# Kernel tuning notes

Hardware: AMD Instinct MI355X
Metric: run time of the kernel (lower is better)

## Reference

```python
import jax, jax.numpy as jnp
import numpy as np

SIGMA = 1.0  # init kwarg sigma

def _rbf_kernel(A):
    # K[i,j] = exp(-0.5 * ||a_i - a_j||^2 / sigma^2)
    sq = jnp.sum(A * A, axis=1)                      # [n]
    d2 = sq[:, None] + sq[None, :] - 2.0 * (A @ A.T)  # [n, n]
    return jnp.exp(-0.5 * d2 / (SIGMA ** 2))

def _double_center(K):
    # C K C with C = I - 11^T/n, done in O(n^2) via mean subtraction
    row = K.mean(axis=1, keepdims=True)
    col = K.mean(axis=0, keepdims=True)
    tot = K.mean()
    return K - row - col + tot

def setup_inputs() -> dict:
    key = jax.random.key(0)
    kx, ky = jax.random.split(key)
    X = jax.random.normal(kx, (4096, 512), dtype=jnp.float32)
    Y = jax.random.normal(ky, (4096, 512), dtype=jnp.float32)
    return {"X": X, "Y": Y}

def reference(X, Y):
    n = X.shape[0]
    KXc = _double_center(_rbf_kernel(X))
    KYc = _double_center(_rbf_kernel(Y))
    # trace(KX C KY C) = sum(center(KX) * center(KY)) since K symmetric, C idempotent
    hsic = jnp.sum(KXc * KYc) / ((n - 1) ** 2)
    return hsic
```

## Files before the change

### kernel.cpp

```cpp
#include <hip/hip_runtime.h>
#include <hip/hip_bf16.h>

namespace {

constexpr int N = 4096;
constexpr int D = 512;
constexpr int BM = 128;
constexpr int BK = 64;
constexpr int KITERS = D / BK;
constexpr int NB = N / BM;
constexpr int NBLK = NB * (NB + 1) / 2;
constexpr int TILEB = BM * BK;
constexpr int PANELB = BM * D;

constexpr size_t OFF_XB  = 0;
constexpr size_t OFF_YB  = (size_t)N * D;
constexpr size_t OFF_SQX = OFF_YB + (size_t)N * D;
constexpr size_t OFF_SQY = OFF_SQX + (size_t)N * 4;
constexpr size_t OFF_SX  = OFF_SQY + (size_t)N * 4;
constexpr size_t OFF_SY  = OFF_SX + (size_t)N * 4;
constexpr size_t OFF_T1  = OFF_SY + (size_t)N * 4;
constexpr size_t WS_NEED = OFF_T1 + 4;


constexpr float D2_SKIP = 240.f;

typedef __attribute__((ext_vector_type(4))) float floatx4;
typedef __attribute__((ext_vector_type(2))) long longx2;

__device__ inline void stage16(const void* g, void* l) {
  __builtin_amdgcn_global_load_lds(
      (const __attribute__((address_space(1))) unsigned int*)g,
      (__attribute__((address_space(3))) unsigned int*)l, 16, 0, 0);
}

__device__ inline unsigned short bf16bits(float f) {
  return __builtin_bit_cast(unsigned short, __float2bfloat16(f));
}

__global__ void prep_kernel(const float* __restrict__ X, const float* __restrict__ Y,
                            unsigned char* __restrict__ Xf8, unsigned char* __restrict__ Yf8,
                            float* __restrict__ sqX, float* __restrict__ sqY,
                            float* __restrict__ sX, float* __restrict__ sY,
                            float* __restrict__ T1) {
  const int wave = threadIdx.x >> 6, lane = threadIdx.x & 63;
  const int row = blockIdx.x * 4 + wave;
  const int m = blockIdx.y;
  const float* __restrict__ src = m ? Y : X;
  unsigned char* __restrict__ dst = m ? Yf8 : Xf8;
  float* __restrict__ dsq = m ? sqY : sqX;

  if (threadIdx.x < 4) {
    float* z = m ? sY : sX;
    z[blockIdx.x * 4 + threadIdx.x] = 0.f;
  }
  if (blockIdx.x == 0 && m == 0 && threadIdx.x == 0) *T1 = 0.f;

  const float4* s4 = (const float4*)(src + (size_t)row * D);
  float4 v0 = s4[lane * 2];
  float4 v1 = s4[lane * 2 + 1];
  float acc = v0.x * v0.x + v0.y * v0.y + v0.z * v0.z + v0.w * v0.w
            + v1.x * v1.x + v1.y * v1.y + v1.z * v1.z + v1.w * v1.w;

  unsigned int w0 = 0, w1 = 0;
  w0 = __builtin_amdgcn_cvt_pk_fp8_f32(v0.x, v0.y, w0, false);
  w0 = __builtin_amdgcn_cvt_pk_fp8_f32(v0.z, v0.w, w0, true);
  w1 = __builtin_amdgcn_cvt_pk_fp8_f32(v1.x, v1.y, w1, false);
  w1 = __builtin_amdgcn_cvt_pk_fp8_f32(v1.z, v1.w, w1, true);
  const unsigned long long pk =
      (unsigned long long)w0 | ((unsigned long long)w1 << 32);

  const int p    = row >> 7;
  const int half = (row >> 6) & 1;
  const int nib  = (row >> 4) & 3;
  const int cl   = row & 15;
  const int ks   = lane >> 3;
  const int pass = (lane >> 2) & 1;
  const int quad = lane & 3;
  const size_t off = (size_t)p * PANELB + (size_t)ks * TILEB +
                     half * 4096 + nib * 1024 + quad * 256 + cl * 16 + pass * 8;
  *(unsigned long long*)(dst + off) = pk;

#pragma unroll
  for (int mm = 32; mm >= 1; mm >>= 1) acc += __shfl_xor(acc, mm, 64);
  if (lane == 0) dsq[row] = acc;
}

__launch_bounds__(256, 3)
__global__ void hsic_main(const unsigned char* __restrict__ Xf8,
                          const unsigned char* __restrict__ Yf8,
                          const float* __restrict__ sqX, const float* __restrict__ sqY,
                          float* __restrict__ sX, float* __restrict__ sY,
                          float* __restrict__ T1) {
  __shared__ __align__(16) unsigned char smem[2][2 * TILEB];

  const int b = blockIdx.x;
  int idx = (b & 7) * (NBLK / 8) + (b >> 3);

  const float nf = (float)NB + 0.5f;
  int bI = (int)(nf - sqrtf(nf * nf - 2.0f * (float)idx));
  if (bI < 0) bI = 0;
  if (bI >= NB) bI = NB - 1;
  while (bI * NB - bI * (bI - 1) / 2 > idx) --bI;
  while ((bI + 1) * NB - (bI + 1) * bI / 2 <= idx) ++bI;
  const int bJ = bI + (idx - (bI * NB - bI * (bI - 1) / 2));
  const bool offdiag = (bI != bJ);

  const int tid = threadIdx.x;
  const int lane = tid & 63, wave = tid >> 6;
  const int wm = wave >> 1, wn = wave & 1;
  const int quad = lane >> 4, cl = lane & 15;

  const unsigned char* gAx = Xf8 + (size_t)bI * PANELB;
  const unsigned char* gBx = Xf8 + (size_t)bJ * PANELB;
  const unsigned char* gAy = Yf8 + (size_t)bI * PANELB;
  const unsigned char* gBy = Yf8 + (size_t)bJ * PANELB;

  floatx4 acc[4][4];
#pragma unroll
  for (int i = 0; i < 4; ++i)
#pragma unroll
    for (int j = 0; j < 4; ++j) acc[i][j] = (floatx4){0.f, 0.f, 0.f, 0.f};

  auto stage_all = [&](int iter, int buf) {
    const unsigned char* gA = (iter < KITERS) ? gAx : gAy;
    const unsigned char* gB = (iter < KITERS) ? gBx : gBy;
    const size_t ks0 = (size_t)(iter & (KITERS - 1)) * TILEB;
#pragma unroll
    for (int h = 0; h < 2; ++h) {
      const int c = tid + h * 256;
      const size_t goff = ks0 + (size_t)c * 16;
      stage16(gA + goff, &smem[buf][0 * TILEB + c * 16]);
      if (offdiag) stage16(gB + goff, &smem[buf][1 * TILEB + c * 16]);
    }
  };

  const int Ib = bI * BM + wm * 64;
  const int Jb = bJ * BM + wn * 64;

  unsigned int kxp[4][4][2];
  unsigned int fmask = 0;
  float t1l = 0.f;

  stage_all(0, 0);

  for (int iter = 0; iter < 2 * KITERS; ++iter) {
    const int buf = iter & 1;
    __syncthreads();
    if (iter + 1 < 2 * KITERS) stage_all(iter + 1, buf ^ 1);

    const unsigned char* A = &smem[buf][0];
    const unsigned char* B = offdiag ? &smem[buf][TILEB] : &smem[buf][0];

    longx2 bf[4];
#pragma unroll
    for (int ni = 0; ni < 4; ++ni)
      bf[ni] = *(const longx2*)&B[wn * 4096 + ni * 1024 + (lane << 4)];
#pragma unroll
    for (int mi = 0; mi < 4; ++mi) {
      const longx2 af = *(const longx2*)&A[wm * 4096 + mi * 1024 + (lane << 4)];
#pragma unroll
      for (int ni = 0; ni < 4; ++ni) {
        acc[mi][ni] = __builtin_amdgcn_mfma_f32_16x16x32_fp8_fp8(af[0], bf[ni][0], acc[mi][ni], 0, 0, 0);
        acc[mi][ni] = __builtin_amdgcn_mfma_f32_16x16x32_fp8_fp8(af[1], bf[ni][1], acc[mi][ni], 0, 0, 0);
      }
    }

    if (iter == KITERS - 1) {
      float rx[4][4];
      float cx[4];
#pragma unroll
      for (int mi = 0; mi < 4; ++mi)
#pragma unroll
        for (int r = 0; r < 4; ++r) rx[mi][r] = 0.f;
#pragma unroll
      for (int ni = 0; ni < 4; ++ni) cx[ni] = 0.f;

#pragma unroll
      for (int mi = 0; mi < 4; ++mi) {
        const int ig0 = Ib + mi * 16 + quad * 4;
        float sxi[4];
#pragma unroll
        for (int r = 0; r < 4; ++r) sxi[r] = sqX[ig0 + r];
#pragma unroll
        for (int ni = 0; ni < 4; ++ni) {
          const int jg = Jb + ni * 16 + cl;
          const float sxj = sqX[jg];
          float d2x[4];
          bool lflag = false;
#pragma unroll
          for (int r = 0; r < 4; ++r) {
            const int ig = ig0 + r;
            d2x[r] = sxi[r] + sxj - 2.f * acc[mi][ni][r];
            lflag |= (d2x[r] < D2_SKIP) | (ig == jg);
          }
          float kxv[4] = {0.f, 0.f, 0.f, 0.f};
          if (__any(lflag)) {
            fmask |= (1u << (mi * 4 + ni));
#pragma unroll
            for (int r = 0; r < 4; ++r) {
              const int ig = ig0 + r;
              kxv[r] = (ig == jg) ? 1.f : __expf(-0.5f * d2x[r]);
              rx[mi][r] += kxv[r];
              cx[ni] += kxv[r];
            }
          }
          kxp[mi][ni][0] = (unsigned)bf16bits(kxv[0]) | ((unsigned)bf16bits(kxv[1]) << 16);
          kxp[mi][ni][1] = (unsigned)bf16bits(kxv[2]) | ((unsigned)bf16bits(kxv[3]) << 16);
          acc[mi][ni] = (floatx4){0.f, 0.f, 0.f, 0.f};
        }
      }

      if (fmask != 0) {
#pragma unroll
        for (int mi = 0; mi < 4; ++mi)
#pragma unroll
          for (int r = 0; r < 4; ++r) {
            float vx = rx[mi][r];
#pragma unroll
            for (int mm = 1; mm < 16; mm <<= 1) vx += __shfl_xor(vx, mm, 16);
            rx[mi][r] = vx;
          }
        if (cl == 0) {
#pragma unroll
          for (int mi = 0; mi < 4; ++mi)
#pragma unroll
            for (int r = 0; r < 4; ++r)
              atomicAdd(&sX[Ib + mi * 16 + quad * 4 + r], rx[mi][r]);
        }
        if (offdiag) {
#pragma unroll
          for (int ni = 0; ni < 4; ++ni) {
            float vx = cx[ni];
            vx += __shfl_xor(vx, 16, 64);
            vx += __shfl_xor(vx, 32, 64);
            if (quad == 0) atomicAdd(&sX[Jb + ni * 16 + cl], vx);
          }
        }
      }
    }
  }

  {
    float ry[4][4];
    float cy[4];
    bool anyy = false;
#pragma unroll
    for (int mi = 0; mi < 4; ++mi)
#pragma unroll
      for (int r = 0; r < 4; ++r) ry[mi][r] = 0.f;
#pragma unroll
    for (int ni = 0; ni < 4; ++ni) cy[ni] = 0.f;

#pragma unroll
    for (int mi = 0; mi < 4; ++mi) {
      const int ig0 = Ib + mi * 16 + quad * 4;
      float syi[4];
#pragma unroll
      for (int r = 0; r < 4; ++r) syi[r] = sqY[ig0 + r];
#pragma unroll
      for (int ni = 0; ni < 4; ++ni) {
        const int jg = Jb + ni * 16 + cl;
        const float syj = sqY[jg];
        float d2y[4];
        bool lflag = false;
#pragma unroll
        for (int r = 0; r < 4; ++r) {
          const int ig = ig0 + r;
          d2y[r] = syi[r] + syj - 2.f * acc[mi][ni][r];
          lflag |= (d2y[r] < D2_SKIP) | (ig == jg);
        }
        const bool xb = (fmask >> (mi * 4 + ni)) & 1u;
        if (__any(lflag) || xb) {
          anyy = true;
          float kyv[4];
#pragma unroll
          for (int r = 0; r < 4; ++r) {
            const int ig = ig0 + r;
            kyv[r] = (ig == jg) ? 1.f : __expf(-0.5f * d2y[r]);
            ry[mi][r] += kyv[r];
            cy[ni] += kyv[r];
          }
          if (xb) {
            const float kx0 = __builtin_bit_cast(float, (kxp[mi][ni][0] & 0xFFFFu) << 16);
            const float kx1 = __builtin_bit_cast(float, kxp[mi][ni][0] & 0xFFFF0000u);
            const float kx2 = __builtin_bit_cast(float, (kxp[mi][ni][1] & 0xFFFFu) << 16);
            const float kx3 = __builtin_bit_cast(float, kxp[mi][ni][1] & 0xFFFF0000u);
            t1l += kx0 * kyv[0] + kx1 * kyv[1] + kx2 * kyv[2] + kx3 * kyv[3];
          }
        }
      }
    }

    if (anyy) {
#pragma unroll
      for (int mi = 0; mi < 4; ++mi)
#pragma unroll
        for (int r = 0; r < 4; ++r) {
          float vy = ry[mi][r];
#pragma unroll
          for (int mm = 1; mm < 16; mm <<= 1) vy += __shfl_xor(vy, mm, 16);
          ry[mi][r] = vy;
        }
      if (cl == 0) {
#pragma unroll
        for (int mi = 0; mi < 4; ++mi)
#pragma unroll
          for (int r = 0; r < 4; ++r)
            atomicAdd(&sY[Ib + mi * 16 + quad * 4 + r], ry[mi][r]);
      }
      if (offdiag) {
#pragma unroll
        for (int ni = 0; ni < 4; ++ni) {
          float vy = cy[ni];
          vy += __shfl_xor(vy, 16, 64);
          vy += __shfl_xor(vy, 32, 64);
          if (quad == 0) atomicAdd(&sY[Jb + ni * 16 + cl], vy);
        }
      }
    }
  }

  if (fmask != 0) {
    t1l *= offdiag ? 2.f : 1.f;
#pragma unroll
    for (int mm = 1; mm < 64; mm <<= 1) t1l += __shfl_xor(t1l, mm, 64);
  }
  __shared__ float tred[4];
  if (lane == 0) tred[wave] = t1l;
  __syncthreads();
  if (tid == 0) {
    const float t = tred[0] + tred[1] + tred[2] + tred[3];
    if (t != 0.f) atomicAdd(T1, t);
  }
}

__global__ void final_kernel(const float* __restrict__ sX, const float* __restrict__ sY,
                             const float* __restrict__ T1, float* __restrict__ out) {
  const int tid = threadIdx.x;
  float dp = 0.f, sa = 0.f, sb = 0.f;
  for (int i = tid; i < N; i += 256) {
    float a = sX[i], b = sY[i];
    dp += a * b; sa += a; sb += b;
  }
#pragma unroll
  for (int mm = 1; mm < 64; mm <<= 1) {
    dp += __shfl_xor(dp, mm, 64);
    sa += __shfl_xor(sa, mm, 64);
    sb += __shfl_xor(sb, mm, 64);
  }
  __shared__ float r0[4], r1[4], r2[4];
  if ((tid & 63) == 0) { int w = tid >> 6; r0[w] = dp; r1[w] = sa; r2[w] = sb; }
  __syncthreads();
  if (tid == 0) {
    dp = r0[0] + r0[1] + r0[2] + r0[3];
    sa = r1[0] + r1[1] + r1[2] + r1[3];
    sb = r2[0] + r2[1] + r2[2] + r2[3];
    const float n = (float)N;
    const float total = T1[0] - (2.f / n) * dp + (sa * sb) / (n * n);
    out[0] = total / ((n - 1.f) * (n - 1.f));
  }
}

}

extern "C" void kernel_launch(void* const* d_in, const int* in_sizes, int n_in,
                              void* d_out, int out_size, void* d_ws, size_t ws_size,
                              hipStream_t stream) {
  const float* X = (const float*)d_in[0];
  const float* Y = (const float*)d_in[1];
  char* ws = (char*)d_ws;
  if (ws_size < WS_NEED) return;

  unsigned char* Xf8 = (unsigned char*)(ws + OFF_XB);
  unsigned char* Yf8 = (unsigned char*)(ws + OFF_YB);
  float* sqX = (float*)(ws + OFF_SQX);
  float* sqY = (float*)(ws + OFF_SQY);
  float* sX  = (float*)(ws + OFF_SX);
  float* sY  = (float*)(ws + OFF_SY);
  float* T1  = (float*)(ws + OFF_T1);
  float* out = (float*)d_out;

  prep_kernel<<<dim3(N / 4, 2), 256, 0, stream>>>(X, Y, Xf8, Yf8, sqX, sqY, sX, sY, T1);
  hsic_main<<<NBLK, 256, 0, stream>>>(Xf8, Yf8, sqX, sqY, sX, sY, T1);
  final_kernel<<<1, 256, 0, stream>>>(sX, sY, T1, out);
}
```

Measured before the change: 96.92 us.

## Stage four K-slices per barrier without double buffering in HSIC main kernel

Replaces the double-buffered 64-wide K pipeline (16 iterations) with 4 iterations that each load 256 bytes of K per row into a single 64KB shared buffer and then compute four slices back to back. This cuts the number of barriers and loop overhead. In exchange, loads no longer overlap with compute, because each iteration waits for its staging to finish. The larger LDS footprint also lowers the launch-bounds occupancy target from 3 to 2 blocks per CU.

```diff
diff --git a/kernel.cpp b/kernel.cpp
--- a/kernel.cpp
+++ b/kernel.cpp
@@ -6,12 +6,12 @@
 constexpr int N = 4096;
 constexpr int D = 512;
 constexpr int BM = 128;
-constexpr int BK = 64;
-constexpr int KITERS = D / BK;
 constexpr int NB = N / BM;
 constexpr int NBLK = NB * (NB + 1) / 2;
-constexpr int TILEB = BM * BK;
+constexpr int TILEB = BM * 64;
 constexpr int PANELB = BM * D;
+constexpr int SLICES = 4;
+constexpr int STAGEB = SLICES * TILEB;
 
 constexpr size_t OFF_XB  = 0;
 constexpr size_t OFF_YB  = (size_t)N * D;
@@ -86,13 +86,14 @@
   if (lane == 0) dsq[row] = acc;
 }
 
-__launch_bounds__(256, 3)
+__launch_bounds__(256, 2)
 __global__ void hsic_main(const unsigned char* __restrict__ Xf8,
                           const unsigned char* __restrict__ Yf8,
                           const float* __restrict__ sqX, const float* __restrict__ sqY,
                           float* __restrict__ sX, float* __restrict__ sY,
                           float* __restrict__ T1) {
-  __shared__ __align__(16) unsigned char smem[2][2 * TILEB];
+  __shared__ __align__(16) unsigned char smem[2 * STAGEB];
+  __shared__ float tred[4];
 
   const int b = blockIdx.x;
   int idx = (b & 7) * (NBLK / 8) + (b >> 3);
@@ -122,16 +123,16 @@
 #pragma unroll
     for (int j = 0; j < 4; ++j) acc[i][j] = (floatx4){0.f, 0.f, 0.f, 0.f};
 
-  auto stage_all = [&](int iter, int buf) {
-    const unsigned char* gA = (iter < KITERS) ? gAx : gAy;
-    const unsigned char* gB = (iter < KITERS) ? gBx : gBy;
-    const size_t ks0 = (size_t)(iter & (KITERS - 1)) * TILEB;
-#pragma unroll
-    for (int h = 0; h < 2; ++h) {
+  auto stage_all = [&](int iter) {
+    const unsigned char* gA = (iter < 2) ? gAx : gAy;
+    const unsigned char* gB = (iter < 2) ? gBx : gBy;
+    const size_t ks0 = (size_t)(iter & 1) * STAGEB;
+#pragma unroll
+    for (int h = 0; h < 8; ++h) {
       const int c = tid + h * 256;
       const size_t goff = ks0 + (size_t)c * 16;
-      stage16(gA + goff, &smem[buf][0 * TILEB + c * 16]);
-      if (offdiag) stage16(gB + goff, &smem[buf][1 * TILEB + c * 16]);
+      stage16(gA + goff, &smem[c * 16]);
+      if (offdiag) stage16(gB + goff, &smem[STAGEB + c * 16]);
     }
   };
 
@@ -142,31 +143,33 @@
   unsigned int fmask = 0;
   float t1l = 0.f;
 
-  stage_all(0, 0);
-
-  for (int iter = 0; iter < 2 * KITERS; ++iter) {
-    const int buf = iter & 1;
+  for (int iter = 0; iter < 4; ++iter) {
+    if (iter > 0) __syncthreads();
+    stage_all(iter);
     __syncthreads();
-    if (iter + 1 < 2 * KITERS) stage_all(iter + 1, buf ^ 1);
-
-    const unsigned char* A = &smem[buf][0];
-    const unsigned char* B = offdiag ? &smem[buf][TILEB] : &smem[buf][0];
-
-    longx2 bf[4];
-#pragma unroll
-    for (int ni = 0; ni < 4; ++ni)
-      bf[ni] = *(const longx2*)&B[wn * 4096 + ni * 1024 + (lane << 4)];
-#pragma unroll
-    for (int mi = 0; mi < 4; ++mi) {
-      const longx2 af = *(const longx2*)&A[wm * 4096 + mi * 1024 + (lane << 4)];
-#pragma unroll
-      for (int ni = 0; ni < 4; ++ni) {
-        acc[mi][ni] = __builtin_amdgcn_mfma_f32_16x16x32_fp8_fp8(af[0], bf[ni][0], acc[mi][ni], 0, 0, 0);
-        acc[mi][ni] = __builtin_amdgcn_mfma_f32_16x16x32_fp8_fp8(af[1], bf[ni][1], acc[mi][ni], 0, 0, 0);
-      }
-    }
-
-    if (iter == KITERS - 1) {
+
+    const unsigned char* A = &smem[0];
+    const unsigned char* B = offdiag ? &smem[STAGEB] : &smem[0];
+
+#pragma unroll
+    for (int s = 0; s < SLICES; ++s) {
+      const int sb = s * TILEB;
+      longx2 bf[4];
+#pragma unroll
+      for (int ni = 0; ni < 4; ++ni)
+        bf[ni] = *(const longx2*)&B[sb + wn * 4096 + ni * 1024 + (lane << 4)];
+#pragma unroll
+      for (int mi = 0; mi < 4; ++mi) {
+        const longx2 af = *(const longx2*)&A[sb + wm * 4096 + mi * 1024 + (lane << 4)];
+#pragma unroll
+        for (int ni = 0; ni < 4; ++ni) {
+          acc[mi][ni] = __builtin_amdgcn_mfma_f32_16x16x32_fp8_fp8(af[0], bf[ni][0], acc[mi][ni], 0, 0, 0);
+          acc[mi][ni] = __builtin_amdgcn_mfma_f32_16x16x32_fp8_fp8(af[1], bf[ni][1], acc[mi][ni], 0, 0, 0);
+        }
+      }
+    }
+
+    if (iter == 1) {
       float rx[4][4];
       float cx[4];
 #pragma unroll
@@ -326,7 +329,6 @@
 #pragma unroll
     for (int mm = 1; mm < 64; mm <<= 1) t1l += __shfl_xor(t1l, mm, 64);
   }
-  __shared__ float tred[4];
   if (lane == 0) tred[wave] = t1l;
   __syncthreads();
   if (tid == 0) {
```

New measurement: 99.82 us. +3.0%, slower.
